# Performance work log

Hardware: AMD Instinct MI355X
Metric: run time of the kernel (lower is better)

Reference implementation:

```python
import jax, jax.numpy as jnp
import numpy as np

B, N, K, C, C_OUT = 8, 4096, 16, 192, 192
BN_EPS = 1e-5


def setup_inputs() -> dict:
    key = jax.random.key(0)
    k1, k2, k3, k4 = jax.random.split(key, 4)
    x = jax.random.normal(k1, (B, N, C), dtype=jnp.float32)
    edge_index = jax.random.randint(k2, (B, N, K), 0, N)
    # Linear(2C -> C_out): store weight as [2C, C_out] (transposed torch layout)
    lim = 1.0 / np.sqrt(2 * C)
    W = jax.random.uniform(k3, (2 * C, C_OUT), minval=-lim, maxval=lim, dtype=jnp.float32)
    b = jax.random.uniform(k4, (C_OUT,), minval=-lim, maxval=lim, dtype=jnp.float32)
    gamma = jnp.ones((C_OUT,), dtype=jnp.float32)
    beta = jnp.zeros((C_OUT,), dtype=jnp.float32)
    return {"x": x, "W": W, "b": b, "gamma": gamma, "beta": beta, "edge_index": edge_index}


def reference(x, W, b, gamma, beta, edge_index):
    Bb, Nn, Cc = x.shape
    # gather neighbor features: neighbors[b,n,k,:] = x[b, edge_index[b,n,k], :]
    batch_idx = jnp.arange(Bb)[:, None, None]          # [B,1,1]
    neighbors = x[batch_idx, edge_index]               # [B,N,K,C]
    # max-relative aggregation: max_k (x_j - x_i)
    agg = jnp.max(neighbors - x[:, :, None, :], axis=2)  # [B,N,C]
    h = jnp.concatenate([x, agg], axis=-1).reshape(Bb * Nn, 2 * Cc)
    # Linear
    y = h @ W + b                                      # [B*N, C_out]
    # BatchNorm1d (training-mode forward: batch stats, biased variance)
    mean = jnp.mean(y, axis=0)
    var = jnp.var(y, axis=0)
    y = (y - mean) * jax.lax.rsqrt(var + BN_EPS) * gamma + beta
    # exact (erf) GELU, torch default
    y = jax.nn.gelu(y, approximate=False)
    return y.reshape(Bb, Nn, -1)
```

## Files before the change

### kernel.cpp

```cpp
#include <hip/hip_runtime.h>
#include <math.h>

#define BDIM 8
#define NDIM 4096
#define KNBR 16
#define CDIM 192
#define COUT 192
#define TWO_C 384
#define ROWS (BDIM * NDIM)
#define BN_EPS 1e-5f

#define BM 64
#define HS 392
#define KSTEPS 12
#define NTILES 12

typedef __attribute__((ext_vector_type(8))) short short8;
typedef __attribute__((ext_vector_type(4))) float f32x4;

__device__ __forceinline__ float bf2f(unsigned short u) {
    unsigned int x = ((unsigned int)u) << 16;
    return __builtin_bit_cast(float, x);
}
__device__ __forceinline__ unsigned short f2bf(float f) {
    unsigned int u = __builtin_bit_cast(unsigned int, f);
    u += 0x7FFFu + ((u >> 16) & 1u);
    return (unsigned short)(u >> 16);
}
__device__ __forceinline__ float gelu_exact(float v) {
    return 0.5f * v * (1.0f + erff(v * 0.70710678118654752440f));
}

#define CVT_BLK0 37
__global__ __launch_bounds__(256)
void prep(const float* __restrict__ x, const float* __restrict__ W,
          unsigned short* __restrict__ xb, unsigned short* __restrict__ Wtp,
          float* __restrict__ stats) {
    const int bid = blockIdx.x;
    const int t   = threadIdx.x;
    if (bid < 36) {
        const int tid = bid * 256 + t;
        const int ks = tid / (NTILES * 64);
        const int r  = tid % (NTILES * 64);
        const int nt = r / 64;
        const int l  = r % 64;
        const int k0 = ks * 32 + ((l >> 4) << 3);
        const int c  = nt * 16 + (l & 15);
        short8 o;
#pragma unroll
        for (int j = 0; j < 8; ++j)
            o[j] = (short)f2bf(W[(size_t)(k0 + j) * COUT + c]);
        *(short8*)(Wtp + (size_t)tid * 8) = o;
        return;
    }
    if (bid == 36) {
        for (int s = t; s < 2 * COUT; s += 256) stats[s] = 0.0f;
        return;
    }
    const int i = (bid - CVT_BLK0) * 256 + t;
    const float4* p = (const float4*)(x + (size_t)i * 8);
    const float4 a = p[0], b = p[1];
    short8 o;
    o[0] = (short)f2bf(a.x); o[1] = (short)f2bf(a.y);
    o[2] = (short)f2bf(a.z); o[3] = (short)f2bf(a.w);
    o[4] = (short)f2bf(b.x); o[5] = (short)f2bf(b.y);
    o[6] = (short)f2bf(b.z); o[7] = (short)f2bf(b.w);
    *(short8*)(xb + (size_t)i * 8) = o;
}

__global__ __launch_bounds__(256)
void mrconv_mfma(const unsigned short* __restrict__ xb,
                 const unsigned short* __restrict__ Wtp,
                 const int*   __restrict__ edge,
                 unsigned short* __restrict__ y,
                 float* __restrict__ stats)
{
    __shared__ unsigned short h[BM * HS];
    __shared__ int eidx[BM * KNBR];

    const int t     = threadIdx.x;
    const int bid   = blockIdx.x;
    const int batch = bid & 7;
    const int tile  = bid >> 3;
    const int row0  = tile * BM;

    const unsigned short* xbb = xb + (size_t)batch * NDIM * CDIM;
    const int* eb = edge + ((size_t)batch * NDIM + row0) * KNBR;

    for (int i = t; i < BM * KNBR; i += 256) eidx[i] = eb[i];
    __syncthreads();

    for (int it = 0; it < 6; ++it) {
        const int idx = it * 256 + t;
        const int cc  = idx % 24;
        const int ln  = idx / 24;
        const short8 xi8 = *(const short8*)(xbb + (size_t)(row0 + ln) * CDIM + cc * 8);
        float mx[8];
#pragma unroll
        for (int q = 0; q < 8; ++q) mx[q] = -INFINITY;
#pragma unroll
        for (int k = 0; k < KNBR; ++k) {
            const int j = eidx[ln * KNBR + k];
            const short8 xj8 = *(const short8*)(xbb + (size_t)j * CDIM + cc * 8);
#pragma unroll
            for (int q = 0; q < 8; ++q)
                mx[q] = fmaxf(mx[q], bf2f((unsigned short)xj8[q]));
        }
        short8 a8;
#pragma unroll
        for (int q = 0; q < 8; ++q)
            a8[q] = (short)f2bf(mx[q] - bf2f((unsigned short)xi8[q]));
        *(short8*)&h[ln * HS + cc * 8]        = xi8;
        *(short8*)&h[ln * HS + CDIM + cc * 8] = a8;
    }
    __syncthreads();

    const int wv   = t >> 6;
    const int lane = t & 63;
    const int lrow = lane & 15;
    const int lk   = (lane >> 4) << 3;

    f32x4 acc[4][3];
#pragma unroll
    for (int mt = 0; mt < 4; ++mt)
#pragma unroll
        for (int nt = 0; nt < 3; ++nt)
            acc[mt][nt] = (f32x4){0.f, 0.f, 0.f, 0.f};

    for (int ks = 0; ks < KSTEPS; ++ks) {
        short8 bfr[3], afr[4];
#pragma unroll
        for (int nt = 0; nt < 3; ++nt) {
            const int ng = wv * 3 + nt;
            bfr[nt] = *(const short8*)(Wtp + (size_t)((ks * NTILES + ng) * 64 + lane) * 8);
        }
#pragma unroll
        for (int mt = 0; mt < 4; ++mt)
            afr[mt] = *(const short8*)&h[(mt * 16 + lrow) * HS + ks * 32 + lk];
#pragma unroll
        for (int mt = 0; mt < 4; ++mt)
#pragma unroll
            for (int nt = 0; nt < 3; ++nt)
                acc[mt][nt] = __builtin_amdgcn_mfma_f32_16x16x32_bf16(
                    afr[mt], bfr[nt], acc[mt][nt], 0, 0, 0);
    }

    const size_t growbase = (size_t)batch * NDIM + row0;
    const int rj = (lane >> 4) << 2;
#pragma unroll
    for (int mt = 0; mt < 4; ++mt) {
#pragma unroll
        for (int nt = 0; nt < 3; ++nt) {
            const int col = wv * 48 + nt * 16 + lrow;
#pragma unroll
            for (int j = 0; j < 4; ++j) {
                const size_t rr = growbase + mt * 16 + rj + j;
                y[rr * COUT + col] = f2bf(acc[mt][nt][j]);
            }
        }
    }

#pragma unroll
    for (int nt = 0; nt < 3; ++nt) {
        float s = 0.f, q = 0.f;
#pragma unroll
        for (int mt = 0; mt < 4; ++mt)
#pragma unroll
            for (int j = 0; j < 4; ++j) {
                const float v = acc[mt][nt][j];
                s += v; q += v * v;
            }
        s += __shfl_xor(s, 16); s += __shfl_xor(s, 32);
        q += __shfl_xor(q, 16); q += __shfl_xor(q, 32);
        if (lane < 16) {
            const int col = wv * 48 + nt * 16 + lane;
            atomicAdd(&stats[col], s);
            atomicAdd(&stats[COUT + col], q);
        }
    }
}

__global__ __launch_bounds__(256)
void bn_gelu(const unsigned short* __restrict__ y,
             const float* __restrict__ stats,
             const float* __restrict__ gamma,
             const float* __restrict__ beta,
             float* __restrict__ out)
{
    __shared__ float sscale[COUT];
    __shared__ float sshift[COUT];
    const int t = threadIdx.x;
    if (t < COUT) {
        const float inv  = 1.0f / (float)ROWS;
        const float mean = stats[t] * inv;
        const float var  = stats[COUT + t] * inv - mean * mean;
        const float rstd = rsqrtf(var + BN_EPS);
        const float sc   = rstd * gamma[t];
        sscale[t] = sc;
        sshift[t] = beta[t] - mean * sc;
    }
    __syncthreads();

    const int i = blockIdx.x * 256 + t;
    short8 v = *(const short8*)(y + (size_t)i * 8);
    const int c0 = (i % 24) * 8;
    float4 o0, o1;
    o0.x = gelu_exact(fmaf(bf2f((unsigned short)v[0]), sscale[c0 + 0], sshift[c0 + 0]));
    o0.y = gelu_exact(fmaf(bf2f((unsigned short)v[1]), sscale[c0 + 1], sshift[c0 + 1]));
    o0.z = gelu_exact(fmaf(bf2f((unsigned short)v[2]), sscale[c0 + 2], sshift[c0 + 2]));
    o0.w = gelu_exact(fmaf(bf2f((unsigned short)v[3]), sscale[c0 + 3], sshift[c0 + 3]));
    o1.x = gelu_exact(fmaf(bf2f((unsigned short)v[4]), sscale[c0 + 4], sshift[c0 + 4]));
    o1.y = gelu_exact(fmaf(bf2f((unsigned short)v[5]), sscale[c0 + 5], sshift[c0 + 5]));
    o1.z = gelu_exact(fmaf(bf2f((unsigned short)v[6]), sscale[c0 + 6], sshift[c0 + 6]));
    o1.w = gelu_exact(fmaf(bf2f((unsigned short)v[7]), sscale[c0 + 7], sshift[c0 + 7]));
    float4* po = (float4*)(out + (size_t)i * 8);
    po[0] = o0;
    po[1] = o1;
}

extern "C" void kernel_launch(void* const* d_in, const int* in_sizes, int n_in,
                              void* d_out, int out_size, void* d_ws, size_t ws_size,
                              hipStream_t stream) {
    const float* x     = (const float*)d_in[0];
    const float* W     = (const float*)d_in[1];
    const float* gamma = (const float*)d_in[3];
    const float* beta  = (const float*)d_in[4];
    const int*   edge  = (const int*)d_in[5];
    float* out = (float*)d_out;

    unsigned short* Wtp  = (unsigned short*)d_ws;
    float* stats = (float*)(Wtp + (size_t)KSTEPS * NTILES * 64 * 8);
    unsigned short* y16  = (unsigned short*)(stats + 2 * COUT);
    unsigned short* xb16 = y16 + (size_t)ROWS * COUT;

    prep<<<dim3(CVT_BLK0 + ROWS * CDIM / 8 / 256), dim3(256), 0, stream>>>(x, W, xb16, Wtp, stats);
    mrconv_mfma<<<dim3(ROWS / BM), dim3(256), 0, stream>>>(xb16, Wtp, edge, y16, stats);
    bn_gelu<<<dim3(ROWS * COUT / 8 / 256), dim3(256), 0, stream>>>(y16, stats, gamma, beta, out);
}
```

Measured before the change: 49.72 us.

## Read x-half of GEMM A from global and batch neighbor gathers

The x_i half of the concatenated activation is no longer staged in LDS. MFMA A-fragments for the first six k-steps are loaded directly from global (L2-resident) bf16 x, which halves LDS usage and should allow more resident blocks. The neighbor gather now issues eight independent 16-byte loads before reducing, instead of a serial load-max chain, to raise memory-level parallelism. The trade-off is extra global loads in the GEMM loop, plus more registers held by the batched gathers.

```diff
diff --git a/kernel.cpp b/kernel.cpp
--- a/kernel.cpp
+++ b/kernel.cpp
@@ -6,21 +6,20 @@
 #define KNBR 16
 #define CDIM 192
 #define COUT 192
-#define TWO_C 384
 #define ROWS (BDIM * NDIM)
 #define BN_EPS 1e-5f
-
-#define BM 64
-#define HS 392
 #define KSTEPS 12
 #define NTILES 12
 
+#define BM 64
+#define AS 200
+
 typedef __attribute__((ext_vector_type(8))) short short8;
 typedef __attribute__((ext_vector_type(4))) float f32x4;
 
 __device__ __forceinline__ float bf2f(unsigned short u) {
-    unsigned int x = ((unsigned int)u) << 16;
-    return __builtin_bit_cast(float, x);
+    unsigned int v = ((unsigned int)u) << 16;
+    return __builtin_bit_cast(float, v);
 }
 __device__ __forceinline__ unsigned short f2bf(float f) {
     unsigned int u = __builtin_bit_cast(unsigned int, f);
@@ -75,8 +74,8 @@
                  unsigned short* __restrict__ y,
                  float* __restrict__ stats)
 {
-    __shared__ unsigned short h[BM * HS];
-    __shared__ int eidx[BM * KNBR];
+    __shared__ __align__(16) unsigned short agg_lds[BM * AS];
+    __shared__ __align__(16) int eidx[BM * KNBR];
 
     const int t     = threadIdx.x;
     const int bid   = blockIdx.x;
@@ -95,23 +94,33 @@
         const int cc  = idx % 24;
         const int ln  = idx / 24;
         const short8 xi8 = *(const short8*)(xbb + (size_t)(row0 + ln) * CDIM + cc * 8);
+
+        short8 xj[8];
         float mx[8];
 #pragma unroll
-        for (int q = 0; q < 8; ++q) mx[q] = -INFINITY;
-#pragma unroll
-        for (int k = 0; k < KNBR; ++k) {
-            const int j = eidx[ln * KNBR + k];
-            const short8 xj8 = *(const short8*)(xbb + (size_t)j * CDIM + cc * 8);
+        for (int k = 0; k < 8; ++k)
+            xj[k] = *(const short8*)(xbb + (size_t)eidx[ln * KNBR + k] * CDIM + cc * 8);
+#pragma unroll
+        for (int q = 0; q < 8; ++q) mx[q] = bf2f((unsigned short)xj[0][q]);
+#pragma unroll
+        for (int k = 1; k < 8; ++k)
 #pragma unroll
             for (int q = 0; q < 8; ++q)
-                mx[q] = fmaxf(mx[q], bf2f((unsigned short)xj8[q]));
-        }
+                mx[q] = fmaxf(mx[q], bf2f((unsigned short)xj[k][q]));
+#pragma unroll
+        for (int k = 0; k < 8; ++k)
+            xj[k] = *(const short8*)(xbb + (size_t)eidx[ln * KNBR + 8 + k] * CDIM + cc * 8);
+#pragma unroll
+        for (int k = 0; k < 8; ++k)
+#pragma unroll
+            for (int q = 0; q < 8; ++q)
+                mx[q] = fmaxf(mx[q], bf2f((unsigned short)xj[k][q]));
+
         short8 a8;
 #pragma unroll
         for (int q = 0; q < 8; ++q)
             a8[q] = (short)f2bf(mx[q] - bf2f((unsigned short)xi8[q]));
-        *(short8*)&h[ln * HS + cc * 8]        = xi8;
-        *(short8*)&h[ln * HS + CDIM + cc * 8] = a8;
+        *(short8*)&agg_lds[ln * AS + cc * 8] = a8;
     }
     __syncthreads();
 
@@ -134,9 +143,15 @@
             const int ng = wv * 3 + nt;
             bfr[nt] = *(const short8*)(Wtp + (size_t)((ks * NTILES + ng) * 64 + lane) * 8);
         }
-#pragma unroll
-        for (int mt = 0; mt < 4; ++mt)
-            afr[mt] = *(const short8*)&h[(mt * 16 + lrow) * HS + ks * 32 + lk];
+        if (ks < 6) {
+#pragma unroll
+            for (int mt = 0; mt < 4; ++mt)
+                afr[mt] = *(const short8*)(xbb + (size_t)(row0 + mt * 16 + lrow) * CDIM + ks * 32 + lk);
+        } else {
+#pragma unroll
+            for (int mt = 0; mt < 4; ++mt)
+                afr[mt] = *(const short8*)&agg_lds[(mt * 16 + lrow) * AS + (ks - 6) * 32 + lk];
+        }
 #pragma unroll
         for (int mt = 0; mt < 4; ++mt)
 #pragma unroll
```

Measured after the change: 53.88 us. +8.4%, slower.
